# Kernel optimization log

Hardware: AMD Instinct MI355X
Metric: run time of the kernel (lower is better)

## Reference

```python
import jax, jax.numpy as jnp
import numpy as np

L, D, H, T, B = 4, 512, 8, 1024, 8
FF = 4 * D          # 2048
E = 2
EC = E * D          # 1024 conv channels
K = 31
W = 64              # attention window
DH = D // H
EPS = 1e-5


def _ln(x, g, b):
    m = jnp.mean(x, axis=-1, keepdims=True)
    v = jnp.mean((x - m) ** 2, axis=-1, keepdims=True)
    return (x - m) * jax.lax.rsqrt(v + EPS) * g + b


def setup_inputs() -> dict:
    key = jax.random.key(0)
    ks = iter(jax.random.split(key, 64))
    n = lambda shape, s=0.02: jax.random.normal(next(ks), shape, dtype=jnp.float32) * s
    inp = {
        'x': jax.random.normal(next(ks), (B, T, D), dtype=jnp.float32),
        # FFN1 (half residual)
        'ffn1_ln_g': jnp.ones((L, D)), 'ffn1_ln_b': jnp.zeros((L, D)),
        'ffn1_w1': n((L, D, FF)), 'ffn1_b1': jnp.zeros((L, FF)),
        'ffn1_w2': n((L, FF, D)), 'ffn1_b2': jnp.zeros((L, D)),
        # local MHSA
        'attn_ln_g': jnp.ones((L, D)), 'attn_ln_b': jnp.zeros((L, D)),
        'qkv_w': n((L, D, 3 * D)), 'qkv_b': jnp.zeros((L, 3 * D)),
        'outp_w': n((L, D, D)), 'outp_b': jnp.zeros((L, D)),
        # conv module
        'conv_ln_g': jnp.ones((L, D)), 'conv_ln_b': jnp.zeros((L, D)),
        'pw1_w': n((L, D, 2 * EC)), 'pw1_b': jnp.zeros((L, 2 * EC)),
        'dw_w': n((L, EC, 1, K), 0.1), 'dw_b': jnp.zeros((L, EC)),
        'gn_g': jnp.ones((L, EC)), 'gn_b': jnp.zeros((L, EC)),
        'pw2_w': n((L, EC, D)), 'pw2_b': jnp.zeros((L, D)),
        # FFN2 (half residual)
        'ffn2_ln_g': jnp.ones((L, D)), 'ffn2_ln_b': jnp.zeros((L, D)),
        'ffn2_w1': n((L, D, FF)), 'ffn2_b1': jnp.zeros((L, FF)),
        'ffn2_w2': n((L, FF, D)), 'ffn2_b2': jnp.zeros((L, D)),
        # per-block final LN and decoder final LN
        'blk_ln_g': jnp.ones((L, D)), 'blk_ln_b': jnp.zeros((L, D)),
        'final_ln_g': jnp.ones((D,)), 'final_ln_b': jnp.zeros((D,)),
    }
    return inp


def _forward(x, ffn1_ln_g, ffn1_ln_b, ffn1_w1, ffn1_b1, ffn1_w2, ffn1_b2,
             attn_ln_g, attn_ln_b, qkv_w, qkv_b, outp_w, outp_b,
             conv_ln_g, conv_ln_b, pw1_w, pw1_b, dw_w, dw_b, gn_g, gn_b, pw2_w, pw2_b,
             ffn2_ln_g, ffn2_ln_b, ffn2_w1, ffn2_b1, ffn2_w2, ffn2_b2,
             blk_ln_g, blk_ln_b, final_ln_g, final_ln_b):
    t = jnp.arange(T)
    local_ok = jnp.abs(t[:, None] - t[None, :]) <= (W // 2)   # [T,T] banded window mask
    scale = DH ** -0.5

    for l in range(L):
        # ---- FFN1 (half residual), SiLU ----
        h = _ln(x, ffn1_ln_g[l], ffn1_ln_b[l])
        h = jax.nn.silu(h @ ffn1_w1[l] + ffn1_b1[l]) @ ffn1_w2[l] + ffn1_b2[l]
        x = x + 0.5 * h

        # ---- local windowed MHSA ----
        a = _ln(x, attn_ln_g[l], attn_ln_b[l])
        qkv = (a @ qkv_w[l] + qkv_b[l]).reshape(B, T, 3, H, DH)
        q, k, v = (qkv[:, :, 0].transpose(0, 2, 1, 3),  # [B,H,T,DH]
                   qkv[:, :, 1].transpose(0, 2, 1, 3),
                   qkv[:, :, 2].transpose(0, 2, 1, 3))
        scores = jnp.einsum('bhqd,bhkd->bhqk', q, k) * scale
        scores = jnp.where(local_ok, scores, -jnp.inf)
        attn = jax.nn.softmax(scores, axis=-1)
        o = jnp.einsum('bhqk,bhkd->bhqd', attn, v)
        o = o.transpose(0, 2, 1, 3).reshape(B, T, D)
        x = x + (o @ outp_w[l] + outp_b[l])

        # ---- convolution module ----
        c = _ln(x, conv_ln_g[l], conv_ln_b[l])
        c = c @ pw1_w[l] + pw1_b[l]                 # [B,T,2EC]
        c = c[..., :EC] * jax.nn.sigmoid(c[..., EC:])  # GLU (channel halves)
        c = c.transpose(0, 2, 1)                    # [B,EC,T]
        c = jax.lax.conv_general_dilated(
            c, dw_w[l], window_strides=(1,), padding=[((K - 1) // 2, (K - 1) // 2)],
            dimension_numbers=('NCH', 'OIH', 'NCH'), feature_group_count=EC)
        c = c + dw_b[l][None, :, None]
        # GroupNorm(num_groups=1): normalize over (C,T) per sample
        m = jnp.mean(c, axis=(1, 2), keepdims=True)
        vv = jnp.mean((c - m) ** 2, axis=(1, 2), keepdims=True)
        c = (c - m) * jax.lax.rsqrt(vv + EPS) * gn_g[l][None, :, None] + gn_b[l][None, :, None]
        c = jax.nn.silu(c)
        c = c.transpose(0, 2, 1) @ pw2_w[l] + pw2_b[l]  # [B,T,D]
        x = x + c

        # ---- FFN2 (half residual) ----
        h = _ln(x, ffn2_ln_g[l], ffn2_ln_b[l])
        h = jax.nn.silu(h @ ffn2_w1[l] + ffn2_b1[l]) @ ffn2_w2[l] + ffn2_b2[l]
        x = x + 0.5 * h

        # ---- per-block final LayerNorm ----
        x = _ln(x, blk_ln_g[l], blk_ln_b[l])

    return _ln(x, final_ln_g, final_ln_b)


def reference(x, ffn1_ln_g, ffn1_ln_b, ffn1_w1, ffn1_b1, ffn1_w2, ffn1_b2,
              attn_ln_g, attn_ln_b, qkv_w, qkv_b, outp_w, outp_b,
              conv_ln_g, conv_ln_b, pw1_w, pw1_b, dw_w, dw_b, gn_g, gn_b, pw2_w, pw2_b,
              ffn2_ln_g, ffn2_ln_b, ffn2_w1, ffn2_b1, ffn2_w2, ffn2_b2,
              blk_ln_g, blk_ln_b, final_ln_g, final_ln_b):
    return _forward(x, ffn1_ln_g, ffn1_ln_b, ffn1_w1, ffn1_b1, ffn1_w2, ffn1_b2,
                    attn_ln_g, attn_ln_b, qkv_w, qkv_b, outp_w, outp_b,
                    conv_ln_g, conv_ln_b, pw1_w, pw1_b, dw_w, dw_b, gn_g, gn_b, pw2_w, pw2_b,
                    ffn2_ln_g, ffn2_ln_b, ffn2_w1, ffn2_b1, ffn2_w2, ffn2_b2,
                    blk_ln_g, blk_ln_b, final_ln_g, final_ln_b)
```

## Files before the change

### kernel.cpp

```cpp
#include <hip/hip_runtime.h>
#include <hip/hip_bf16.h>
#include <math.h>

#define L_ 4
#define D_ 512
#define H_ 8
#define T_ 1024
#define B_ 8
#define FF_ 2048
#define EC_ 1024
#define KW_ 31
#define DH_ 64
#define ROWS (B_*T_)

typedef __attribute__((ext_vector_type(8))) short short8;
typedef __attribute__((ext_vector_type(4))) float f32x4;
typedef __attribute__((ext_vector_type(4))) unsigned short ushort4v;

static __device__ __forceinline__ unsigned short f2bf(float f) {
  __hip_bfloat16 h = __float2bfloat16(f);
  unsigned short u;
  __builtin_memcpy(&u, &h, 2);
  return u;
}
static __device__ __forceinline__ float bf2f(unsigned short h) {
  union { unsigned u; float f; } v; v.u = ((unsigned)h) << 16;
  return v.f;
}
static __device__ __forceinline__ float sigm(float x) {
  return __builtin_amdgcn_rcpf(1.0f + __expf(-x));
}

#define GLDS(gp, lp) __builtin_amdgcn_global_load_lds( \
    (const __attribute__((address_space(1))) unsigned int*)(const void*)(gp), \
    (__attribute__((address_space(3))) unsigned int*)(void*)(lp), 16, 0, 0)

#define SW8(row, slot) ((slot) ^ (((row) ^ ((row) >> 3)) & 7))

__global__ __launch_bounds__(256) void cvt_kernel(const float* __restrict__ in,
                                                  unsigned short* __restrict__ out)
{
  size_t i = ((size_t)blockIdx.x * 256 + threadIdx.x) * 8;
  float4 v0 = *(const float4*)(in + i);
  float4 v1 = *(const float4*)(in + i + 4);
  float vv[8] = {v0.x, v0.y, v0.z, v0.w, v1.x, v1.y, v1.z, v1.w};
  short8 o;
#pragma unroll
  for (int j = 0; j < 8; ++j) o[j] = (short)f2bf(vv[j]);
  *(short8*)(out + i) = o;
}

__global__ __launch_bounds__(256) void ln_bf16_kernel(const unsigned short* __restrict__ x,
    const float* __restrict__ g, const float* __restrict__ b, unsigned short* __restrict__ y)
{
  int row = blockIdx.x * 4 + (threadIdx.x >> 6);
  int l = threadIdx.x & 63;
  short8 xr = *(const short8*)(x + (size_t)row * D_ + l * 8);
  float vv[8];
#pragma unroll
  for (int j = 0; j < 8; ++j) vv[j] = bf2f((unsigned short)xr[j]);
  float s = 0.f, s2 = 0.f;
#pragma unroll
  for (int j = 0; j < 8; ++j) { s += vv[j]; s2 += vv[j] * vv[j]; }
#pragma unroll
  for (int off = 32; off; off >>= 1) {
    s  += __shfl_xor(s,  off, 64);
    s2 += __shfl_xor(s2, off, 64);
  }
  float mean = s * (1.0f / D_);
  float var  = s2 * (1.0f / D_) - mean * mean;
  float r = __builtin_amdgcn_rsqf(var + 1e-5f);
  float4 g0 = *(const float4*)(g + l * 8);
  float4 g1 = *(const float4*)(g + l * 8 + 4);
  float4 b0 = *(const float4*)(b + l * 8);
  float4 b1 = *(const float4*)(b + l * 8 + 4);
  float gg[8] = {g0.x, g0.y, g0.z, g0.w, g1.x, g1.y, g1.z, g1.w};
  float bb[8] = {b0.x, b0.y, b0.z, b0.w, b1.x, b1.y, b1.z, b1.w};
  short8 o;
#pragma unroll
  for (int j = 0; j < 8; ++j) o[j] = (short)f2bf((vv[j] - mean) * r * gg[j] + bb[j]);
  *(short8*)(y + (size_t)row * D_ + l * 8) = o;
}

template<bool BF2>
__global__ __launch_bounds__(256) void ln_dual_kernel(const unsigned short* __restrict__ x,
    const float* __restrict__ g1, const float* __restrict__ b1,
    const float* __restrict__ g2, const float* __restrict__ b2,
    unsigned short* __restrict__ y1, void* __restrict__ y2)
{
  int row = blockIdx.x * 4 + (threadIdx.x >> 6);
  int l = threadIdx.x & 63;
  short8 xr = *(const short8*)(x + (size_t)row * D_ + l * 8);
  float vv[8];
#pragma unroll
  for (int j = 0; j < 8; ++j) vv[j] = bf2f((unsigned short)xr[j]);
  float s = 0.f, s2 = 0.f;
#pragma unroll
  for (int j = 0; j < 8; ++j) { s += vv[j]; s2 += vv[j] * vv[j]; }
#pragma unroll
  for (int off = 32; off; off >>= 1) {
    s  += __shfl_xor(s,  off, 64);
    s2 += __shfl_xor(s2, off, 64);
  }
  float mean = s * (1.0f / D_);
  float var  = s2 * (1.0f / D_) - mean * mean;
  float r = __builtin_amdgcn_rsqf(var + 1e-5f);
  float4 g0 = *(const float4*)(g1 + l * 8);
  float4 g1v = *(const float4*)(g1 + l * 8 + 4);
  float4 b0 = *(const float4*)(b1 + l * 8);
  float4 b1v = *(const float4*)(b1 + l * 8 + 4);
  float ga[8] = {g0.x, g0.y, g0.z, g0.w, g1v.x, g1v.y, g1v.z, g1v.w};
  float ba[8] = {b0.x, b0.y, b0.z, b0.w, b1v.x, b1v.y, b1v.z, b1v.w};
  float yv[8];
  float u = 0.f, u2 = 0.f;
#pragma unroll
  for (int j = 0; j < 8; ++j) {
    yv[j] = (vv[j] - mean) * r * ga[j] + ba[j];
    u += yv[j]; u2 += yv[j] * yv[j];
  }
  {
    short8 o;
#pragma unroll
    for (int j = 0; j < 8; ++j) o[j] = (short)f2bf(yv[j]);
    *(short8*)(y1 + (size_t)row * D_ + l * 8) = o;
  }
#pragma unroll
  for (int off = 32; off; off >>= 1) {
    u  += __shfl_xor(u,  off, 64);
    u2 += __shfl_xor(u2, off, 64);
  }
  float mean2 = u * (1.0f / D_);
  float var2  = u2 * (1.0f / D_) - mean2 * mean2;
  float r2 = __builtin_amdgcn_rsqf(var2 + 1e-5f);
  float4 c0 = *(const float4*)(g2 + l * 8);
  float4 c1 = *(const float4*)(g2 + l * 8 + 4);
  float4 d0 = *(const float4*)(b2 + l * 8);
  float4 d1 = *(const float4*)(b2 + l * 8 + 4);
  float gc[8] = {c0.x, c0.y, c0.z, c0.w, c1.x, c1.y, c1.z, c1.w};
  float bc[8] = {d0.x, d0.y, d0.z, d0.w, d1.x, d1.y, d1.z, d1.w};
  if constexpr (BF2) {
    short8 o;
#pragma unroll
    for (int j = 0; j < 8; ++j) o[j] = (short)f2bf((yv[j] - mean2) * r2 * gc[j] + bc[j]);
    *(short8*)((unsigned short*)y2 + (size_t)row * D_ + l * 8) = o;
  } else {
    float z[8];
#pragma unroll
    for (int j = 0; j < 8; ++j) z[j] = (yv[j] - mean2) * r2 * gc[j] + bc[j];
    float4 o0 = {z[0], z[1], z[2], z[3]};
    float4 o1 = {z[4], z[5], z[6], z[7]};
    float* yp = (float*)y2 + (size_t)row * D_ + l * 8;
    *(float4*)yp = o0; *(float4*)(yp + 4) = o1;
  }
}

__global__ __launch_bounds__(256) void wtr_kernel(const float* __restrict__ W,
    unsigned short* __restrict__ Wt, int K, int N)
{
  __shared__ float tile[32][33];
  const float* Wl = W + (size_t)blockIdx.z * K * N;
  unsigned short* Wtl = Wt + (size_t)blockIdx.z * K * N;
  int n0 = blockIdx.x * 32, k0 = blockIdx.y * 32;
  int c = threadIdx.x & 31, r = threadIdx.x >> 5;
#pragma unroll
  for (int it = 0; it < 4; ++it) {
    int kk = r + it * 8;
    tile[kk][c] = Wl[(size_t)(k0 + kk) * N + n0 + c];
  }
  __syncthreads();
#pragma unroll
  for (int it = 0; it < 4; ++it) {
    int nn = r + it * 8;
    Wtl[(size_t)(n0 + nn) * K + k0 + c] = f2bf(tile[c][nn]);
  }
}

template<int EPI>
__global__ __launch_bounds__(256) void gemm_mfma(
    const unsigned short* __restrict__ A, const unsigned short* __restrict__ Wt,
    const float* __restrict__ bias, void* __restrict__ Cv,
    int N, int K)
{
  constexpr int TM = 128;
  constexpr int AI = TM / 32;
  __shared__ __align__(16) unsigned short As[3][TM * 32];
  __shared__ __align__(16) unsigned short Bs[3][128 * 32];
  int t = threadIdx.x;
  int gx = gridDim.x;
  int nwg = gx * gridDim.y;
  int orig = blockIdx.y * gx + blockIdx.x;
  int lg = (orig & 7) * (nwg >> 3) + (orig >> 3);
  int row0 = (lg / gx) * TM;
  int col0 = (lg % gx) * (EPI == 3 ? 64 : 128);
  int l = t & 63, w = t >> 6, wm = w >> 1, wn = w & 1;

  int ar0 = t >> 2;
  int sa0 = (t & 3) ^ ((ar0 >> 1) & 3);
  int ar1 = (t + 256) >> 2;
  int sa1 = (t & 3) ^ ((ar1 >> 1) & 3);
  const unsigned short* agp0 = A + (size_t)(row0 + ar0) * K + sa0 * 8;
  const unsigned short* agp1 = A + (size_t)(row0 + ar1) * K + sa1 * 8;
  const unsigned short* bgp0 = Wt + (size_t)(col0 + ar0) * K + sa0 * 8;
  const unsigned short* bgp1 =
      (EPI == 3) ? Wt + (size_t)(EC_ + col0 + (ar1 - 64)) * K + sa1 * 8
                 : Wt + (size_t)(col0 + ar1) * K + sa1 * 8;

  int lrow = (l >> 4) * 4, lcol = l & 15, kq = l >> 4;
  int aoff[AI], boff[4];
#pragma unroll
  for (int i = 0; i < AI; ++i) {
    int row = wm * (TM / 2) + i * 16 + lcol;
    aoff[i] = (row * 4 + (kq ^ ((row >> 1) & 3))) * 8;
  }
#pragma unroll
  for (int j = 0; j < 4; ++j) {
    int row;
    if constexpr (EPI == 3)
      row = (j < 2 ? wn * 32 + j * 16 : 64 + wn * 32 + (j - 2) * 16) + lcol;
    else
      row = wn * 64 + j * 16 + lcol;
    boff[j] = (row * 4 + (kq ^ ((row >> 1) & 3))) * 8;
  }

  f32x4 acc[AI][4] = {};
  int nt = K >> 5;

  auto stage = [&](int buf) {
    GLDS(agp0, As[buf] + t * 8);
    GLDS(agp1, As[buf] + (t + 256) * 8);
    GLDS(bgp0, Bs[buf] + t * 8);
    GLDS(bgp1, Bs[buf] + (t + 256) * 8);
    agp0 += 32; agp1 += 32; bgp0 += 32; bgp1 += 32;
  };
  stage(0); stage(1);
  int cur = 0, nxt = 2;

  for (int kt = 0; kt < nt; ++kt) {
    if (kt < nt - 1) asm volatile("s_waitcnt vmcnt(4)" ::: "memory");
    else             asm volatile("s_waitcnt vmcnt(0)" ::: "memory");
    __builtin_amdgcn_s_barrier();
    __builtin_amdgcn_sched_barrier(0);
    if (kt + 2 < nt) { stage(nxt); nxt = (nxt == 2) ? 0 : nxt + 1; }
    const unsigned short* Ab = As[cur];
    const unsigned short* Bb = Bs[cur];
    cur = (cur == 2) ? 0 : cur + 1;
    short8 af[AI], bfr[4];
#pragma unroll
    for (int i = 0; i < AI; ++i) af[i]  = *(const short8*)(Ab + aoff[i]);
#pragma unroll
    for (int j = 0; j < 4; ++j) bfr[j] = *(const short8*)(Bb + boff[j]);
    __builtin_amdgcn_s_setprio(1);
#pragma unroll
    for (int i = 0; i < AI; ++i)
#pragma unroll
      for (int j = 0; j < 4; ++j)
        acc[i][j] = __builtin_amdgcn_mfma_f32_16x16x32_bf16(af[i], bfr[j], acc[i][j], 0, 0, 0);
    __builtin_amdgcn_s_setprio(0);
  }

  if constexpr (EPI == 3) {
    float bja[2], bjg[2];
#pragma unroll
    for (int j = 0; j < 2; ++j) {
      int c = col0 + wn * 32 + j * 16 + lcol;
      bja[j] = bias[c];
      bjg[j] = bias[EC_ + c];
    }
#pragma unroll
    for (int i = 0; i < AI; ++i) {
      int gr0 = row0 + wm * (TM / 2) + i * 16 + lrow;
#pragma unroll
      for (int j = 0; j < 2; ++j) {
        int gc = col0 + wn * 32 + j * 16 + lcol;
#pragma unroll
        for (int q = 0; q < 4; ++q) {
          float a = acc[i][j][q] + bja[j];
          float g = acc[i][j + 2][q] + bjg[j];
          ((unsigned short*)Cv)[(size_t)(gr0 + q) * N + gc] = f2bf(a * sigm(g));
        }
      }
    }
  } else {
    float bj[4];
#pragma unroll
    for (int j = 0; j < 4; ++j) bj[j] = bias[col0 + wn * 64 + j * 16 + lcol];
#pragma unroll
    for (int i = 0; i < AI; ++i) {
      int gr0 = row0 + wm * (TM / 2) + i * 16 + lrow;
#pragma unroll
      for (int j = 0; j < 4; ++j) {
        int gc = col0 + wn * 64 + j * 16 + lcol;
#pragma unroll
        for (int q = 0; q < 4; ++q) {
          float v = acc[i][j][q] + bj[j];
          size_t off = (size_t)(gr0 + q) * N + gc;
          if constexpr (EPI == 0) {
            ((unsigned short*)Cv)[off] = f2bf(v);
          } else {
            ((unsigned short*)Cv)[off] = f2bf(v * sigm(v));
          }
        }
      }
    }
  }
}

__global__ __launch_bounds__(256) void gemm_res64(
    const unsigned short* __restrict__ A, const unsigned short* __restrict__ Wt,
    const float* __restrict__ bias, const unsigned short* __restrict__ R,
    unsigned short* __restrict__ C, int N, int K, float alpha)
{
  __shared__ __align__(16) unsigned short As[3][64 * 64];
  __shared__ __align__(16) unsigned short Bs[3][128 * 64];
  int t = threadIdx.x;
  int gx = gridDim.x;
  int nwg = gx * gridDim.y;
  int orig = blockIdx.y * gx + blockIdx.x;
  int lg = (orig & 7) * (nwg >> 3) + (orig >> 3);
  int row0 = (lg / gx) * 64;
  int col0 = (lg % gx) * 128;
  int l = t & 63, w = t >> 6, wm = w >> 1, wn = w & 1;

  int arA0 = t >> 3;
  int sA0  = (t & 7) ^ (arA0 & 7);
  int cA1  = t + 256;
  int arA1 = cA1 >> 3;
  int sA1  = (cA1 & 7) ^ (arA1 & 7);
  const unsigned short* agp0 = A + (size_t)(row0 + arA0) * K + sA0 * 8;
  const unsigned short* agp1 = A + (size_t)(row0 + arA1) * K + sA1 * 8;
  const unsigned short* bgp[4];
#pragma unroll
  for (int q = 0; q < 4; ++q) {
    int c = t + q * 256;
    int r = c >> 3, s = (c & 7) ^ (r & 7);
    bgp[q] = Wt + (size_t)(col0 + r) * K + s * 8;
  }

  int lcol = l & 15, kq = l >> 4, lrow = kq * 4;
  int aoff[2][2], boff[4][2];
#pragma unroll
  for (int i = 0; i < 2; ++i) {
    int row = wm * 32 + i * 16 + lcol;
#pragma unroll
    for (int kk = 0; kk < 2; ++kk)
      aoff[i][kk] = row * 64 + (((kk * 4 + kq) ^ (row & 7)) * 8);
  }
#pragma unroll
  for (int j = 0; j < 4; ++j) {
    int row = wn * 64 + j * 16 + lcol;
#pragma unroll
    for (int kk = 0; kk < 2; ++kk)
      boff[j][kk] = row * 64 + (((kk * 4 + kq) ^ (row & 7)) * 8);
  }

  f32x4 acc[2][4] = {};
  int nt = K >> 6;

  auto stage = [&](int buf) {
    GLDS(agp0, As[buf] + t * 8);
    GLDS(agp1, As[buf] + (t + 256) * 8);
#pragma unroll
    for (int q = 0; q < 4; ++q) GLDS(bgp[q], Bs[buf] + (t + q * 256) * 8);
    agp0 += 64; agp1 += 64;
#pragma unroll
    for (int q = 0; q < 4; ++q) bgp[q] += 64;
  };
  stage(0); stage(1);
  int cur = 0, nxt = 2;

  for (int kt = 0; kt < nt; ++kt) {
    if (kt < nt - 1) asm volatile("s_waitcnt vmcnt(6)" ::: "memory");
    else             asm volatile("s_waitcnt vmcnt(0)" ::: "memory");
    __builtin_amdgcn_s_barrier();
    __builtin_amdgcn_sched_barrier(0);
    if (kt + 2 < nt) { stage(nxt); nxt = (nxt == 2) ? 0 : nxt + 1; }
    const unsigned short* Ab = As[cur];
    const unsigned short* Bb = Bs[cur];
    cur = (cur == 2) ? 0 : cur + 1;
    short8 af[2][2], bfr[4][2];
#pragma unroll
    for (int i = 0; i < 2; ++i)
#pragma unroll
      for (int kk = 0; kk < 2; ++kk) af[i][kk] = *(const short8*)(Ab + aoff[i][kk]);
#pragma unroll
    for (int j = 0; j < 4; ++j)
#pragma unroll
      for (int kk = 0; kk < 2; ++kk) bfr[j][kk] = *(const short8*)(Bb + boff[j][kk]);
    __builtin_amdgcn_s_setprio(1);
#pragma unroll
    for (int kk = 0; kk < 2; ++kk)
#pragma unroll
      for (int i = 0; i < 2; ++i)
#pragma unroll
        for (int j = 0; j < 4; ++j)
          acc[i][j] = __builtin_amdgcn_mfma_f32_16x16x32_bf16(af[i][kk], bfr[j][kk],
                                                              acc[i][j], 0, 0, 0);
    __builtin_amdgcn_s_setprio(0);
  }

  float bj[4];
#pragma unroll
  for (int j = 0; j < 4; ++j) bj[j] = bias[col0 + wn * 64 + j * 16 + lcol];
#pragma unroll
  for (int i = 0; i < 2; ++i) {
    int gr0 = row0 + wm * 32 + i * 16 + lrow;
#pragma unroll
    for (int j = 0; j < 4; ++j) {
      int gc = col0 + wn * 64 + j * 16 + lcol;
#pragma unroll
      for (int q = 0; q < 4; ++q) {
        size_t off = (size_t)(gr0 + q) * N + gc;
        C[off] = f2bf(bf2f(R[off]) + alpha * (acc[i][j][q] + bj[j]));
      }
    }
  }
}

__global__ __launch_bounds__(256) void attn_kernel(const unsigned short* __restrict__ QKV,
                                                   unsigned short* __restrict__ O)
{
  __shared__ __align__(16) unsigned short Ks[128 * 64];
  __shared__ __align__(16) unsigned short Vt[64 * 128];
  __shared__ __align__(16) unsigned short Ps[64 * 128];
  int qt = blockIdx.x, h = blockIdx.y, b = blockIdx.z;
  int t = threadIdx.x;
  int l = t & 63, w = t >> 6;
  int q0 = qt * 64;
  int jbase = q0 - 32;

#pragma unroll
  for (int i = 0; i < 4; ++i) {
    int c = t + i * 256;
    int row = c >> 3, sl = c & 7;
    int jg = jbase + row;
    short8 kv = {};
    if ((unsigned)jg < (unsigned)T_)
      kv = *(const short8*)(QKV + ((size_t)(b * T_ + jg)) * 1536 + 512 + h * DH_ + sl * 8);
    *(short8*)(Ks + row * 64 + SW8(row, sl) * 8) = kv;
  }
#pragma unroll
  for (int i = 0; i < 4; ++i) {
    int c = t + i * 256;
    int row = c >> 3, d0 = (c & 7) * 8;
    int jg = jbase + row;
    short8 vv = {};
    if ((unsigned)jg < (unsigned)T_)
      vv = *(const short8*)(QKV + ((size_t)(b * T_ + jg)) * 1536 + 1024 + h * DH_ + d0);
#pragma unroll
    for (int q = 0; q < 8; ++q) {
      int d = d0 + q;
      Vt[d * 128 + SW8(d, row >> 3) * 8 + (row & 7)] = (unsigned short)vv[q];
    }
  }
  short8 qf[2];
#pragma unroll
  for (int ks = 0; ks < 2; ++ks)
    qf[ks] = *(const short8*)(QKV + ((size_t)(b * T_ + q0 + w * 16 + (l & 15))) * 1536
                              + h * DH_ + ks * 32 + (l >> 4) * 8);
  __syncthreads();

  f32x4 sacc[8] = {};
#pragma unroll
  for (int jt = 0; jt < 8; ++jt) {
#pragma unroll
    for (int ks = 0; ks < 2; ++ks) {
      int row = jt * 16 + (l & 15);
      int sl = ks * 4 + (l >> 4);
      short8 kf = *(const short8*)(Ks + row * 64 + SW8(row, sl) * 8);
      sacc[jt] = __builtin_amdgcn_mfma_f32_16x16x32_bf16(qf[ks], kf, sacc[jt], 0, 0, 0);
    }
  }

  const float scale = 0.125f;
  int qgl0 = q0 + w * 16 + ((l >> 4) << 2);
  int jl = jbase + (l & 15);
  float m4[4] = {-3.0e38f, -3.0e38f, -3.0e38f, -3.0e38f};
#pragma unroll
  for (int jt = 0; jt < 8; ++jt) {
#pragma unroll
    for (int r = 0; r < 4; ++r) {
      float s = sacc[jt][r] * scale;
      int jg = jl + jt * 16;
      int dd = jg - (qgl0 + r);
      bool ok = ((unsigned)jg < (unsigned)T_) && (dd <= 32) && (dd >= -32);
      s = ok ? s : -3.0e38f;
      sacc[jt][r] = s;
      m4[r] = fmaxf(m4[r], s);
    }
  }
#pragma unroll
  for (int r = 0; r < 4; ++r) {
    m4[r] = fmaxf(m4[r], __shfl_xor(m4[r], 1, 64));
    m4[r] = fmaxf(m4[r], __shfl_xor(m4[r], 2, 64));
    m4[r] = fmaxf(m4[r], __shfl_xor(m4[r], 4, 64));
    m4[r] = fmaxf(m4[r], __shfl_xor(m4[r], 8, 64));
  }
  float sum4[4] = {0.f, 0.f, 0.f, 0.f};
#pragma unroll
  for (int jt = 0; jt < 8; ++jt) {
#pragma unroll
    for (int r = 0; r < 4; ++r) {
      float e = __expf(sacc[jt][r] - m4[r]);
      sum4[r] += e;
      int qrow = w * 16 + ((l >> 4) << 2) + r;
      int j = jt * 16 + (l & 15);
      Ps[qrow * 128 + SW8(qrow, j >> 3) * 8 + (j & 7)] = f2bf(e);
    }
  }
#pragma unroll
  for (int r = 0; r < 4; ++r) {
    sum4[r] += __shfl_xor(sum4[r], 1, 64);
    sum4[r] += __shfl_xor(sum4[r], 2, 64);
    sum4[r] += __shfl_xor(sum4[r], 4, 64);
    sum4[r] += __shfl_xor(sum4[r], 8, 64);
    sum4[r] = __builtin_amdgcn_rcpf(sum4[r]);
  }

  f32x4 oacc[4] = {};
#pragma unroll
  for (int ks = 0; ks < 4; ++ks) {
    int prow = w * 16 + (l & 15);
    int sl = ks * 4 + (l >> 4);
    short8 pf = *(const short8*)(Ps + prow * 128 + SW8(prow, sl) * 8);
#pragma unroll
    for (int dt = 0; dt < 4; ++dt) {
      int vrow = dt * 16 + (l & 15);
      short8 vf = *(const short8*)(Vt + vrow * 128 + SW8(vrow, sl) * 8);
      oacc[dt] = __builtin_amdgcn_mfma_f32_16x16x32_bf16(pf, vf, oacc[dt], 0, 0, 0);
    }
  }
#pragma unroll
  for (int dt = 0; dt < 4; ++dt) {
#pragma unroll
    for (int r = 0; r < 4; ++r) {
      int qg = q0 + w * 16 + ((l >> 4) << 2) + r;
      int d = dt * 16 + (l & 15);
      O[((size_t)(b * T_ + qg)) * D_ + h * DH_ + d] = f2bf(oacc[dt][r] * sum4[r]);
    }
  }
}

#define TT_ 16
__global__ __launch_bounds__(256) void dwconv_kernel(const unsigned short* __restrict__ X,
    const float* __restrict__ w, const float* __restrict__ bias,
    unsigned short* __restrict__ Y, float* __restrict__ red)
{
  int t = threadIdx.x;
  int gid = blockIdx.x;
  int ecb = gid & 3;
  int tt  = (gid >> 2) & 63;
  int b   = gid >> 8;
  int e  = ecb * 256 + t;
  int t0 = tt * TT_;
  const unsigned short* xp = X + (size_t)b * T_ * EC_ + e;

  float wr[KW_];
#pragma unroll
  for (int k = 0; k < KW_; ++k) wr[k] = w[e * KW_ + k];
  float out[TT_];
  float bv = bias[e];
#pragma unroll
  for (int i = 0; i < TT_; ++i) out[i] = bv;

#pragma unroll
  for (int j = 0; j < TT_ + KW_ - 1; ++j) {
    int tj = t0 - 15 + j;
    float xv = ((unsigned)tj < (unsigned)T_) ? bf2f(xp[(size_t)tj * EC_]) : 0.f;
#pragma unroll
    for (int i = 0; i < TT_; ++i) {
      int k = j - i;
      if (k >= 0 && k < KW_) out[i] = fmaf(xv, wr[k], out[i]);
    }
  }
  unsigned short* yp = Y + ((size_t)b * T_ + t0) * EC_ + e;
  float s = 0.f, s2 = 0.f;
#pragma unroll
  for (int i = 0; i < TT_; ++i) {
    yp[(size_t)i * EC_] = f2bf(out[i]);
    s += out[i]; s2 += out[i] * out[i];
  }
#pragma unroll
  for (int off = 32; off; off >>= 1) {
    s  += __shfl_down(s,  off, 64);
    s2 += __shfl_down(s2, off, 64);
  }
  __shared__ float rs[4], rq[4];
  if ((t & 63) == 0) { rs[t >> 6] = s; rq[t >> 6] = s2; }
  __syncthreads();
  if (t == 0) {
    int loc = gid & 255;
    red[(b * 256 + loc) * 2]     = rs[0] + rs[1] + rs[2] + rs[3];
    red[(b * 256 + loc) * 2 + 1] = rq[0] + rq[1] + rq[2] + rq[3];
  }
}

__global__ __launch_bounds__(256) void gn_stats_kernel(const float* __restrict__ partial,
                                                       float* __restrict__ stats)
{
  int b = blockIdx.x, t = threadIdx.x;
  float s  = partial[b * 512 + t * 2];
  float s2 = partial[b * 512 + t * 2 + 1];
#pragma unroll
  for (int off = 32; off; off >>= 1) {
    s  += __shfl_down(s,  off, 64);
    s2 += __shfl_down(s2, off, 64);
  }
  __shared__ float rs[4], rq[4];
  if ((t & 63) == 0) { rs[t >> 6] = s; rq[t >> 6] = s2; }
  __syncthreads();
  if (t == 0) {
    float S = rs[0] + rs[1] + rs[2] + rs[3];
    float S2 = rq[0] + rq[1] + rq[2] + rq[3];
    const float n = (float)(T_ * EC_);
    float mean = S / n;
    float var  = S2 / n - mean * mean;
    stats[b * 2]     = mean;
    stats[b * 2 + 1] = __builtin_amdgcn_rsqf(var + 1e-5f);
  }
}

__global__ __launch_bounds__(256) void gn_apply_kernel(const unsigned short* __restrict__ X,
    const float* __restrict__ stats, const float* __restrict__ g, const float* __restrict__ bb,
    unsigned short* __restrict__ out)
{
  int idx = blockIdx.x * 256 + threadIdx.x;
  int e4 = (idx & 255) << 2;
  int bt = idx >> 8;
  int b  = bt >> 10;
  float mean = stats[b * 2], rstd = stats[b * 2 + 1];
  ushort4v v = *(const ushort4v*)(X + (size_t)idx * 4);
  float4 gv = *(const float4*)(g + e4);
  float4 bv = *(const float4*)(bb + e4);
  float gg[4] = {gv.x, gv.y, gv.z, gv.w};
  float bbv[4] = {bv.x, bv.y, bv.z, bv.w};
  ushort4v o;
#pragma unroll
  for (int j = 0; j < 4; ++j) {
    float u = (bf2f(v[j]) - mean) * rstd * gg[j] + bbv[j];
    o[j] = f2bf(u * sigm(u));
  }
  *(ushort4v*)(out + (size_t)idx * 4) = o;
}

extern "C" void kernel_launch(void* const* d_in, const int* in_sizes, int n_in,
                              void* d_out, int out_size, void* d_ws, size_t ws_size,
                              hipStream_t stream)
{
  const float* in_x      = (const float*)d_in[0];
  const float* ffn1_ln_g = (const float*)d_in[1];
  const float* ffn1_ln_b = (const float*)d_in[2];
  const float* ffn1_w1   = (const float*)d_in[3];
  const float* ffn1_b1   = (const float*)d_in[4];
  const float* ffn1_w2   = (const float*)d_in[5];
  const float* ffn1_b2   = (const float*)d_in[6];
  const float* attn_ln_g = (const float*)d_in[7];
  const float* attn_ln_b = (const float*)d_in[8];
  const float* qkv_w     = (const float*)d_in[9];
  const float* qkv_b     = (const float*)d_in[10];
  const float* outp_w    = (const float*)d_in[11];
  const float* outp_b    = (const float*)d_in[12];
  const float* conv_ln_g = (const float*)d_in[13];
  const float* conv_ln_b = (const float*)d_in[14];
  const float* pw1_w     = (const float*)d_in[15];
  const float* pw1_b     = (const float*)d_in[16];
  const float* dw_w      = (const float*)d_in[17];
  const float* dw_b      = (const float*)d_in[18];
  const float* gn_g      = (const float*)d_in[19];
  const float* gn_b      = (const float*)d_in[20];
  const float* pw2_w     = (const float*)d_in[21];
  const float* pw2_b     = (const float*)d_in[22];
  const float* ffn2_ln_g = (const float*)d_in[23];
  const float* ffn2_ln_b = (const float*)d_in[24];
  const float* ffn2_w1   = (const float*)d_in[25];
  const float* ffn2_b1   = (const float*)d_in[26];
  const float* ffn2_w2   = (const float*)d_in[27];
  const float* ffn2_b2   = (const float*)d_in[28];
  const float* blk_ln_g  = (const float*)d_in[29];
  const float* blk_ln_b  = (const float*)d_in[30];
  const float* fin_ln_g  = (const float*)d_in[31];
  const float* fin_ln_b  = (const float*)d_in[32];

  char* p = (char*)d_ws;
  unsigned short* x    = (unsigned short*)p; p += (size_t)ROWS * D_ * 2;
  unsigned short* big3 = (unsigned short*)p; p += (size_t)ROWS * EC_ * 2;
  float* red  = (float*)p;          p += 8192 * 4;
  unsigned short* abuf  = (unsigned short*)p; p += (size_t)ROWS * D_ * 2;
  unsigned short* inner = (unsigned short*)p; p += (size_t)ROWS * FF_ * 2;
  unsigned short* big2  = (unsigned short*)p; p += (size_t)ROWS * EC_ * 2;
  unsigned short* wt_w1a = (unsigned short*)p; p += (size_t)L_ * D_ * FF_ * 2;
  unsigned short* wt_w1b = (unsigned short*)p; p += (size_t)L_ * FF_ * D_ * 2;
  unsigned short* wt_qkv = (unsigned short*)p; p += (size_t)L_ * D_ * 1536 * 2;
  unsigned short* wt_out = (unsigned short*)p; p += (size_t)L_ * D_ * D_ * 2;
  unsigned short* wt_pw1 = (unsigned short*)p; p += (size_t)L_ * D_ * 2048 * 2;
  unsigned short* wt_pw2 = (unsigned short*)p; p += (size_t)L_ * EC_ * D_ * 2;
  unsigned short* wt_w2a = (unsigned short*)p; p += (size_t)L_ * D_ * FF_ * 2;
  unsigned short* wt_w2b = (unsigned short*)p; p += (size_t)L_ * FF_ * D_ * 2;
  float* stats = red + 4096;

  dim3 blk256(256);
  cvt_kernel<<<ROWS * D_ / (256 * 8), blk256, 0, stream>>>(in_x, x);

  wtr_kernel<<<dim3(FF_/32,  D_/32,  L_), blk256, 0, stream>>>(ffn1_w1, wt_w1a, D_, FF_);
  wtr_kernel<<<dim3(D_/32,   FF_/32, L_), blk256, 0, stream>>>(ffn1_w2, wt_w1b, FF_, D_);
  wtr_kernel<<<dim3(1536/32, D_/32,  L_), blk256, 0, stream>>>(qkv_w,   wt_qkv, D_, 1536);
  wtr_kernel<<<dim3(D_/32,   D_/32,  L_), blk256, 0, stream>>>(outp_w,  wt_out, D_, D_);
  wtr_kernel<<<dim3(2048/32, D_/32,  L_), blk256, 0, stream>>>(pw1_w,   wt_pw1, D_, 2048);
  wtr_kernel<<<dim3(D_/32,   EC_/32, L_), blk256, 0, stream>>>(pw2_w,   wt_pw2, EC_, D_);
  wtr_kernel<<<dim3(FF_/32,  D_/32,  L_), blk256, 0, stream>>>(ffn2_w1, wt_w2a, D_, FF_);
  wtr_kernel<<<dim3(D_/32,   FF_/32, L_), blk256, 0, stream>>>(ffn2_w2, wt_w2b, FF_, D_);

  ln_bf16_kernel<<<ROWS/4, blk256, 0, stream>>>(x, ffn1_ln_g, ffn1_ln_b, abuf);

  for (int l = 0; l < L_; ++l) {
    gemm_mfma<1><<<dim3(FF_/128, ROWS/128), blk256, 0, stream>>>(
        abuf, wt_w1a + (size_t)l*D_*FF_, ffn1_b1 + l*FF_, inner, FF_, D_);
    gemm_res64<<<dim3(D_/128, ROWS/64), blk256, 0, stream>>>(
        inner, wt_w1b + (size_t)l*FF_*D_, ffn1_b2 + l*D_, x, x, D_, FF_, 0.5f);

    ln_bf16_kernel<<<ROWS/4, blk256, 0, stream>>>(x, attn_ln_g + l*D_, attn_ln_b + l*D_, abuf);
    gemm_mfma<0><<<dim3(1536/128, ROWS/128), blk256, 0, stream>>>(
        abuf, wt_qkv + (size_t)l*D_*1536, qkv_b + l*1536, inner, 1536, D_);
    attn_kernel<<<dim3(T_/64, H_, B_), blk256, 0, stream>>>(inner, abuf);
    gemm_res64<<<dim3(D_/128, ROWS/64), blk256, 0, stream>>>(
        abuf, wt_out + (size_t)l*D_*D_, outp_b + l*D_, x, x, D_, D_, 1.0f);

    ln_bf16_kernel<<<ROWS/4, blk256, 0, stream>>>(x, conv_ln_g + l*D_, conv_ln_b + l*D_, abuf);
    gemm_mfma<3><<<dim3(EC_/64, ROWS/128), blk256, 0, stream>>>(
        abuf, wt_pw1 + (size_t)l*D_*2048, pw1_b + l*2048, big2, EC_, D_);
    dwconv_kernel<<<B_ * (T_/TT_) * (EC_/256), blk256, 0, stream>>>(
        big2, dw_w + (size_t)l*EC_*KW_, dw_b + l*EC_, big3, red);
    gn_stats_kernel<<<B_, blk256, 0, stream>>>(red, stats);
    gn_apply_kernel<<<(ROWS * EC_ / 4) / 256, blk256, 0, stream>>>(
        big3, stats, gn_g + l*EC_, gn_b + l*EC_, big2);
    gemm_res64<<<dim3(D_/128, ROWS/64), blk256, 0, stream>>>(
        big2, wt_pw2 + (size_t)l*EC_*D_, pw2_b + l*D_, x, x, D_, EC_, 1.0f);

    ln_bf16_kernel<<<ROWS/4, blk256, 0, stream>>>(x, ffn2_ln_g + l*D_, ffn2_ln_b + l*D_, abuf);
    gemm_mfma<1><<<dim3(FF_/128, ROWS/128), blk256, 0, stream>>>(
        abuf, wt_w2a + (size_t)l*D_*FF_, ffn2_b1 + l*FF_, inner, FF_, D_);
    gemm_res64<<<dim3(D_/128, ROWS/64), blk256, 0, stream>>>(
        inner, wt_w2b + (size_t)l*FF_*D_, ffn2_b2 + l*D_, x, x, D_, FF_, 0.5f);

    if (l < L_ - 1) {
      ln_dual_kernel<true><<<ROWS/4, blk256, 0, stream>>>(
          x, blk_ln_g + l*D_, blk_ln_b + l*D_,
          ffn1_ln_g + (l+1)*D_, ffn1_ln_b + (l+1)*D_, x, abuf);
    } else {
      ln_dual_kernel<false><<<ROWS/4, blk256, 0, stream>>>(
          x, blk_ln_g + l*D_, blk_ln_b + l*D_, fin_ln_g, fin_ln_b, x, d_out);
    }
  }
}
```

Baseline: 1.150 ms.

## Enlarge residual GEMM tile to 128x128 with 512 threads; widen dwconv per thread

The residual-output GEMM moves from a 64x128 tile on 256 threads to a 128x128 tile on 512 threads (8 waves), with each thread issuing two A and two B global-to-LDS loads per stage. The point is more reuse of each weight tile and fewer workgroups. The depthwise conv now handles two adjacent channels per thread using 2-wide bf16 loads and stores, which halves the block count, and the GroupNorm partial reduction is resized to match. The trade-off is 96KB of LDS per block and twice the registers per thread in dwconv, which may hurt occupancy, plus only 256 blocks for the N=512 GEMMs.

Measured after the change: 1.189 ms. +3.4%, slower.

```diff
diff --git a/kernel.cpp b/kernel.cpp
--- a/kernel.cpp
+++ b/kernel.cpp
@@ -16,6 +16,7 @@
 typedef __attribute__((ext_vector_type(8))) short short8;
 typedef __attribute__((ext_vector_type(4))) float f32x4;
 typedef __attribute__((ext_vector_type(4))) unsigned short ushort4v;
+typedef __attribute__((ext_vector_type(2))) unsigned short ushort2v;
 
 static __device__ __forceinline__ unsigned short f2bf(float f) {
   __hip_bfloat16 h = __float2bfloat16(f);
@@ -305,36 +306,30 @@
   }
 }
 
-__global__ __launch_bounds__(256) void gemm_res64(
+__global__ __launch_bounds__(512) void gemm_res128(
     const unsigned short* __restrict__ A, const unsigned short* __restrict__ Wt,
     const float* __restrict__ bias, const unsigned short* __restrict__ R,
     unsigned short* __restrict__ C, int N, int K, float alpha)
 {
-  __shared__ __align__(16) unsigned short As[3][64 * 64];
+  __shared__ __align__(16) unsigned short As[3][128 * 64];
   __shared__ __align__(16) unsigned short Bs[3][128 * 64];
   int t = threadIdx.x;
   int gx = gridDim.x;
   int nwg = gx * gridDim.y;
   int orig = blockIdx.y * gx + blockIdx.x;
   int lg = (orig & 7) * (nwg >> 3) + (orig >> 3);
-  int row0 = (lg / gx) * 64;
+  int row0 = (lg / gx) * 128;
   int col0 = (lg % gx) * 128;
   int l = t & 63, w = t >> 6, wm = w >> 1, wn = w & 1;
 
-  int arA0 = t >> 3;
-  int sA0  = (t & 7) ^ (arA0 & 7);
-  int cA1  = t + 256;
-  int arA1 = cA1 >> 3;
-  int sA1  = (cA1 & 7) ^ (arA1 & 7);
-  const unsigned short* agp0 = A + (size_t)(row0 + arA0) * K + sA0 * 8;
-  const unsigned short* agp1 = A + (size_t)(row0 + arA1) * K + sA1 * 8;
-  const unsigned short* bgp[4];
-#pragma unroll
-  for (int q = 0; q < 4; ++q) {
-    int c = t + q * 256;
-    int r = c >> 3, s = (c & 7) ^ (r & 7);
-    bgp[q] = Wt + (size_t)(col0 + r) * K + s * 8;
-  }
+  int rA0 = t >> 3;
+  int s0  = (t & 7) ^ (rA0 & 7);
+  int rA1 = (t + 512) >> 3;
+  int s1  = ((t + 512) & 7) ^ (rA1 & 7);
+  const unsigned short* agp0 = A + (size_t)(row0 + rA0) * K + s0 * 8;
+  const unsigned short* agp1 = A + (size_t)(row0 + rA1) * K + s1 * 8;
+  const unsigned short* bgp0 = Wt + (size_t)(col0 + rA0) * K + s0 * 8;
+  const unsigned short* bgp1 = Wt + (size_t)(col0 + rA1) * K + s1 * 8;
 
   int lcol = l & 15, kq = l >> 4, lrow = kq * 4;
   int aoff[2][2], boff[4][2];
@@ -358,18 +353,16 @@
 
   auto stage = [&](int buf) {
     GLDS(agp0, As[buf] + t * 8);
-    GLDS(agp1, As[buf] + (t + 256) * 8);
-#pragma unroll
-    for (int q = 0; q < 4; ++q) GLDS(bgp[q], Bs[buf] + (t + q * 256) * 8);
-    agp0 += 64; agp1 += 64;
-#pragma unroll
-    for (int q = 0; q < 4; ++q) bgp[q] += 64;
+    GLDS(agp1, As[buf] + (t + 512) * 8);
+    GLDS(bgp0, Bs[buf] + t * 8);
+    GLDS(bgp1, Bs[buf] + (t + 512) * 8);
+    agp0 += 64; agp1 += 64; bgp0 += 64; bgp1 += 64;
   };
   stage(0); stage(1);
   int cur = 0, nxt = 2;
 
   for (int kt = 0; kt < nt; ++kt) {
-    if (kt < nt - 1) asm volatile("s_waitcnt vmcnt(6)" ::: "memory");
+    if (kt < nt - 1) asm volatile("s_waitcnt vmcnt(4)" ::: "memory");
     else             asm volatile("s_waitcnt vmcnt(0)" ::: "memory");
     __builtin_amdgcn_s_barrier();
     __builtin_amdgcn_sched_barrier(0);
@@ -547,37 +540,46 @@
 {
   int t = threadIdx.x;
   int gid = blockIdx.x;
-  int ecb = gid & 3;
-  int tt  = (gid >> 2) & 63;
-  int b   = gid >> 8;
-  int e  = ecb * 256 + t;
+  int ecb = gid & 1;
+  int tt  = (gid >> 1) & 63;
+  int b   = gid >> 7;
+  int e0 = ecb * 512 + t * 2;
   int t0 = tt * TT_;
-  const unsigned short* xp = X + (size_t)b * T_ * EC_ + e;
-
-  float wr[KW_];
-#pragma unroll
-  for (int k = 0; k < KW_; ++k) wr[k] = w[e * KW_ + k];
-  float out[TT_];
-  float bv = bias[e];
-#pragma unroll
-  for (int i = 0; i < TT_; ++i) out[i] = bv;
+  const unsigned short* xp = X + (size_t)b * T_ * EC_ + e0;
+
+  float wr0[KW_], wr1[KW_];
+#pragma unroll
+  for (int k = 0; k < KW_; ++k) { wr0[k] = w[e0 * KW_ + k]; wr1[k] = w[(e0 + 1) * KW_ + k]; }
+  float out0[TT_], out1[TT_];
+  float bv0 = bias[e0], bv1 = bias[e0 + 1];
+#pragma unroll
+  for (int i = 0; i < TT_; ++i) { out0[i] = bv0; out1[i] = bv1; }
 
 #pragma unroll
   for (int j = 0; j < TT_ + KW_ - 1; ++j) {
     int tj = t0 - 15 + j;
-    float xv = ((unsigned)tj < (unsigned)T_) ? bf2f(xp[(size_t)tj * EC_]) : 0.f;
+    float x0 = 0.f, x1 = 0.f;
+    if ((unsigned)tj < (unsigned)T_) {
+      ushort2v u = *(const ushort2v*)(xp + (size_t)tj * EC_);
+      x0 = bf2f(u.x); x1 = bf2f(u.y);
+    }
 #pragma unroll
     for (int i = 0; i < TT_; ++i) {
       int k = j - i;
-      if (k >= 0 && k < KW_) out[i] = fmaf(xv, wr[k], out[i]);
-    }
-  }
-  unsigned short* yp = Y + ((size_t)b * T_ + t0) * EC_ + e;
+      if (k >= 0 && k < KW_) {
+        out0[i] = fmaf(x0, wr0[k], out0[i]);
+        out1[i] = fmaf(x1, wr1[k], out1[i]);
+      }
+    }
+  }
+  unsigned short* yp = Y + ((size_t)b * T_ + t0) * EC_ + e0;
   float s = 0.f, s2 = 0.f;
 #pragma unroll
   for (int i = 0; i < TT_; ++i) {
-    yp[(size_t)i * EC_] = f2bf(out[i]);
-    s += out[i]; s2 += out[i] * out[i];
+    ushort2v o; o.x = f2bf(out0[i]); o.y = f2bf(out1[i]);
+    *(ushort2v*)(yp + (size_t)i * EC_) = o;
+    s += out0[i] + out1[i];
+    s2 += out0[i] * out0[i] + out1[i] * out1[i];
   }
 #pragma unroll
   for (int off = 32; off; off >>= 1) {
@@ -588,9 +590,9 @@
   if ((t & 63) == 0) { rs[t >> 6] = s; rq[t >> 6] = s2; }
   __syncthreads();
   if (t == 0) {
-    int loc = gid & 255;
-    red[(b * 256 + loc) * 2]     = rs[0] + rs[1] + rs[2] + rs[3];
-    red[(b * 256 + loc) * 2 + 1] = rq[0] + rq[1] + rq[2] + rq[3];
+    int loc = gid & 127;
+    red[(b * 128 + loc) * 2]     = rs[0] + rs[1] + rs[2] + rs[3];
+    red[(b * 128 + loc) * 2 + 1] = rq[0] + rq[1] + rq[2] + rq[3];
   }
 }
 
@@ -598,8 +600,11 @@
                                                        float* __restrict__ stats)
 {
   int b = blockIdx.x, t = threadIdx.x;
-  float s  = partial[b * 512 + t * 2];
-  float s2 = partial[b * 512 + t * 2 + 1];
+  float s = 0.f, s2 = 0.f;
+  if (t < 128) {
+    s  = partial[b * 256 + t * 2];
+    s2 = partial[b * 256 + t * 2 + 1];
+  }
 #pragma unroll
   for (int off = 32; off; off >>= 1) {
     s  += __shfl_down(s,  off, 64);
@@ -714,31 +719,31 @@
   for (int l = 0; l < L_; ++l) {
     gemm_mfma<1><<<dim3(FF_/128, ROWS/128), blk256, 0, stream>>>(
         abuf, wt_w1a + (size_t)l*D_*FF_, ffn1_b1 + l*FF_, inner, FF_, D_);
-    gemm_res64<<<dim3(D_/128, ROWS/64), blk256, 0, stream>>>(
+    gemm_res128<<<dim3(D_/128, ROWS/128), 512, 0, stream>>>(
         inner, wt_w1b + (size_t)l*FF_*D_, ffn1_b2 + l*D_, x, x, D_, FF_, 0.5f);
 
     ln_bf16_kernel<<<ROWS/4, blk256, 0, stream>>>(x, attn_ln_g + l*D_, attn_ln_b + l*D_, abuf);
     gemm_mfma<0><<<dim3(1536/128, ROWS/128), blk256, 0, stream>>>(
         abuf, wt_qkv + (size_t)l*D_*1536, qkv_b + l*1536, inner, 1536, D_);
     attn_kernel<<<dim3(T_/64, H_, B_), blk256, 0, stream>>>(inner, abuf);
-    gemm_res64<<<dim3(D_/128, ROWS/64), blk256, 0, stream>>>(
+    gemm_res128<<<dim3(D_/128, ROWS/128), 512, 0, stream>>>(
         abuf, wt_out + (size_t)l*D_*D_, outp_b + l*D_, x, x, D_, D_, 1.0f);
 
     ln_bf16_kernel<<<ROWS/4, blk256, 0, stream>>>(x, conv_ln_g + l*D_, conv_ln_b + l*D_, abuf);
     gemm_mfma<3><<<dim3(EC_/64, ROWS/128), blk256, 0, stream>>>(
         abuf, wt_pw1 + (size_t)l*D_*2048, pw1_b + l*2048, big2, EC_, D_);
-    dwconv_kernel<<<B_ * (T_/TT_) * (EC_/256), blk256, 0, stream>>>(
+    dwconv_kernel<<<B_ * (T_/TT_) * (EC_/512), blk256, 0, stream>>>(
         big2, dw_w + (size_t)l*EC_*KW_, dw_b + l*EC_, big3, red);
     gn_stats_kernel<<<B_, blk256, 0, stream>>>(red, stats);
     gn_apply_kernel<<<(ROWS * EC_ / 4) / 256, blk256, 0, stream>>>(
         big3, stats, gn_g + l*EC_, gn_b + l*EC_, big2);
-    gemm_res64<<<dim3(D_/128, ROWS/64), blk256, 0, stream>>>(
+    gemm_res128<<<dim3(D_/128, ROWS/128), 512, 0, stream>>>(
         big2, wt_pw2 + (size_t)l*EC_*D_, pw2_b + l*D_, x, x, D_, EC_, 1.0f);
 
     ln_bf16_kernel<<<ROWS/4, blk256, 0, stream>>>(x, ffn2_ln_g + l*D_, ffn2_ln_b + l*D_, abuf);
     gemm_mfma<1><<<dim3(FF_/128, ROWS/128), blk256, 0, stream>>>(
         abuf, wt_w2a + (size_t)l*D_*FF_, ffn2_b1 + l*FF_, inner, FF_, D_);
-    gemm_res64<<<dim3(D_/128, ROWS/64), blk256, 0, stream>>>(
+    gemm_res128<<<dim3(D_/128, ROWS/128), 512, 0, stream>>>(
         inner, wt_w2b + (size_t)l*FF_*D_, ffn2_b2 + l*D_, x, x, D_, FF_, 0.5f);
 
     if (l < L_ - 1) {
```
